# Optimization experiments

Measured on AMD Instinct MI355X. Metric: run time of the kernel, lower is better.

Reference implementation:

```python
import jax, jax.numpy as jnp
import numpy as np

CAPS_N, DIMS_N, ROUNDS = 10, 16, 3
IN_CAPS_N, IN_DIMS_N = 1152, 8
BATCH = 256
EPS = 1e-7  # keras backend.epsilon()


def squash(x, axis=-1):
    sq = jnp.sum(x * x, axis=axis, keepdims=True)
    return (sq / (1.0 + sq)) * x / jnp.sqrt(sq + EPS)


def setup_inputs() -> dict:
    key = jax.random.key(0)
    k1, k2 = jax.random.split(key)
    inputs = jax.random.normal(k1, (BATCH, IN_CAPS_N, IN_DIMS_N), dtype=jnp.float32)
    # glorot-ish scale for the transform weights
    W = jax.random.normal(k2, (CAPS_N, IN_CAPS_N, DIMS_N, IN_DIMS_N), dtype=jnp.float32) * 0.05
    return {"inputs": inputs, "W": W}


def reference(inputs, W):
    # u_hat[b,j,i,d] = W[j,i] @ inputs[b,i]  (per-pair prediction vectors)
    u_hat = jnp.einsum('jide,bie->bjid', W, inputs)  # [B, caps_n, in_caps_n, dims_n]
    B = inputs.shape[0]
    cc = jnp.zeros((B, CAPS_N, IN_CAPS_N), dtype=u_hat.dtype)  # routing logits
    v = None
    for r in range(ROUNDS):
        c = jax.nn.softmax(cc, axis=1)                    # softmax over output capsules
        s = jnp.einsum('bji,bjid->bjd', c, u_hat)         # weighted sum over input caps
        v = squash(s, axis=-1)                            # [B, caps_n, dims_n]
        if r != ROUNDS - 1:
            cc = cc + jnp.einsum('bjid,bjd->bji', u_hat, v)  # agreement
    return v
```

## Files before the change

### kernel.cpp

```cpp
#include <hip/hip_runtime.h>

#define B_N 256
#define IC_N 1152
#define J_N 10
#define D_N 16

typedef __attribute__((ext_vector_type(8))) short short8;
typedef __attribute__((ext_vector_type(4))) float floatx4;

union u4s8 { uint4 u; short8 s; };

__device__ __forceinline__ float bf_lo(unsigned int u){
  union { unsigned int i; float f; } c; c.i = u << 16; return c.f;
}
__device__ __forceinline__ float bf_hi(unsigned int u){
  union { unsigned int i; float f; } c; c.i = u & 0xffff0000u; return c.f;
}
__device__ __forceinline__ unsigned int rne16(float f){
  union { float ff; unsigned int i; } c; c.ff = f;
  return (c.i + 0x7FFFu + ((c.i >> 16) & 1u)) >> 16;
}
__device__ __forceinline__ unsigned int pack_rne(float lo, float hi){
  return rne16(lo) | (rne16(hi) << 16);
}
__device__ __forceinline__ unsigned int pack_trunc(float lo, float hi){
  union { float f; unsigned int u; } a, b; a.f = lo; b.f = hi;
  return __builtin_amdgcn_perm(b.u, a.u, 0x07060302u);
}

__global__ __launch_bounds__(256) void caps_prep(
    const float* __restrict__ W, const float* __restrict__ x,
    uint4* __restrict__ wsf, uint4* __restrict__ wcc2,
    uint4* __restrict__ xbf_ib, uint4* __restrict__ xbf_bi,
    float* __restrict__ vsum)
{
  const int tid = threadIdx.x;
  if (blockIdx.x < 720) {
    __shared__ unsigned int lw[1024];
    const int j = blockIdx.x / 72, itile = blockIdx.x % 72;
    const float4* Wt = (const float4*)(W + ((size_t)(j * IC_N + itile * 16) << 7));
    #pragma unroll
    for (int h = 0; h < 2; ++h) {
      const float4 f = Wt[h * 256 + tid];
      lw[(h * 256 + tid) * 2]     = pack_rne(f.x, f.y);
      lw[(h * 256 + tid) * 2 + 1] = pack_rne(f.z, f.w);
    }
    __syncthreads();
    {
      const int ktl = tid >> 6, lane = tid & 63;
      const int base = (ktl * 4 + (lane >> 4)) * 64 + (lane & 15) * 4;
      uint4 q;
      q.x = lw[base]; q.y = lw[base + 1]; q.z = lw[base + 2]; q.w = lw[base + 3];
      wsf[((size_t)j * 288 + itile * 4 + ktl) * 64 + lane] = q;
    }
    {
      const int e = tid >> 5, lane2 = tid & 31;
      const int il = lane2 & 15, dbase = (lane2 >> 4) * 8;
      unsigned short h[8];
      #pragma unroll
      for (int k = 0; k < 8; ++k) {
        const unsigned int u = lw[il * 64 + (dbase + k) * 4 + (e >> 1)];
        h[k] = (e & 1) ? (unsigned short)(u >> 16) : (unsigned short)(u & 0xffffu);
      }
      uint4 q;
      q.x = h[0] | ((unsigned int)h[1] << 16);
      q.y = h[2] | ((unsigned int)h[3] << 16);
      q.z = h[4] | ((unsigned int)h[5] << 16);
      q.w = h[6] | ((unsigned int)h[7] << 16);
      wcc2[(((size_t)j * 8 + e) * 72 + itile) * 32 + lane2] = q;
    }
  } else {
    __shared__ unsigned int tx[4][64 * 17];
    const int xb = blockIdx.x - 720;
    const int t0 = xb * 256 + tid;
    if (t0 < B_N * J_N * D_N) vsum[t0] = 0.f;
    const int b0 = (xb / 18) * 16;
    const int i0 = (xb % 18) * 64;
    #pragma unroll
    for (int r = 0; r < 4; ++r) {
      const int bl = r * 4 + (tid >> 6);
      const int il = tid & 63;
      const float4* sp = (const float4*)(x + ((size_t)((b0 + bl) * IC_N + i0 + il) << 3));
      const float4 a = sp[0], c = sp[1];
      uint4 q;
      q.x = pack_rne(a.x, a.y); q.y = pack_rne(a.z, a.w);
      q.z = pack_rne(c.x, c.y); q.w = pack_rne(c.z, c.w);
      xbf_bi[(size_t)(b0 + bl) * IC_N + i0 + il] = q;
      tx[0][il * 17 + bl] = q.x; tx[1][il * 17 + bl] = q.y;
      tx[2][il * 17 + bl] = q.z; tx[3][il * 17 + bl] = q.w;
    }
    __syncthreads();
    #pragma unroll
    for (int it = 0; it < 4; ++it) {
      const int p  = it * 256 + tid;
      const int il = p >> 4, bl = p & 15;
      uint4 q;
      q.x = tx[0][il * 17 + bl]; q.y = tx[1][il * 17 + bl];
      q.z = tx[2][il * 17 + bl]; q.w = tx[3][il * 17 + bl];
      xbf_ib[(size_t)(i0 + il) * 256 + b0 + bl] = q;
    }
  }
}

__global__ __launch_bounds__(640, 5) void caps_pass(
    const uint4* __restrict__ xbf_ib,
    const uint4* __restrict__ xbf_bi,
    const uint4* __restrict__ wsf,
    const uint4* __restrict__ wcc2,
    const uint4* __restrict__ vsbf,
    float* __restrict__ s_part,
    const int round)
{
  __shared__ float ccl[10 * 16 * 17];

  const int tid  = threadIdx.x;
  const int wave = tid >> 6;
  const int lane = tid & 63;
  const int quad = lane >> 4;
  const int col  = lane & 15;
  const int b0   = blockIdx.x << 4;
  const int i0   = blockIdx.y << 4;

  if (round > 0) {
    short8 av = {0,0,0,0,0,0,0,0};
    if (quad < 2)
      av = *(const short8*)&vsbf[((size_t)(b0 + col) * J_N + wave) * 2 + quad];

    uint4 bvq[8];
    #pragma unroll
    for (int e = 0; e < 8; ++e) {
      uint4 q = {0u, 0u, 0u, 0u};
      if (lane < 32)
        q = wcc2[(((size_t)wave * 8 + e) * 72 + blockIdx.y) * 32 + lane];
      bvq[e] = q;
    }
    uint4 xr[4];
    #pragma unroll
    for (int r = 0; r < 4; ++r)
      xr[r] = xbf_bi[(size_t)(b0 + quad * 4 + r) * IC_N + i0 + col];

    floatx4 cc4 = {0.f, 0.f, 0.f, 0.f};
    #pragma unroll
    for (int e = 0; e < 8; ++e) {
      u4s8 bv; bv.u = bvq[e];
      floatx4 tf = {0.f, 0.f, 0.f, 0.f};
      tf = __builtin_amdgcn_mfma_f32_16x16x32_bf16(av, bv.s, tf, 0, 0, 0);
      #pragma unroll
      for (int r = 0; r < 4; ++r) {
        const unsigned int u = ((const unsigned int*)&xr[r])[e >> 1];
        const float xe = (e & 1) ? bf_hi(u) : bf_lo(u);
        cc4[r] += tf[r] * xe;
      }
    }
    #pragma unroll
    for (int r = 0; r < 4; ++r)
      ccl[(wave * 16 + col) * 17 + quad * 4 + r] = cc4[r];
    __syncthreads();
    if (tid < 256) {
      const int i = tid >> 4, b = tid & 15;
      float cc[10];
      #pragma unroll
      for (int j = 0; j < 10; ++j) cc[j] = ccl[(j * 16 + i) * 17 + b];
      float m = cc[0];
      #pragma unroll
      for (int j = 1; j < 10; ++j) m = fmaxf(m, cc[j]);
      float den = 0.f;
      #pragma unroll
      for (int j = 0; j < 10; ++j) { cc[j] = __expf(cc[j] - m); den += cc[j]; }
      const float rd = __builtin_amdgcn_rcpf(den);
      #pragma unroll
      for (int j = 0; j < 10; ++j) ccl[(j * 16 + i) * 17 + b] = cc[j] * rd;
    }
    __syncthreads();
  }

  floatx4 acc = {0.f, 0.f, 0.f, 0.f};
  uint4 xq[4], wf[4];
  float cv[4];
  #pragma unroll
  for (int kt = 0; kt < 4; ++kt) {
    const int il = kt * 4 + quad;
    xq[kt] = xbf_ib[(size_t)(i0 + il) * 256 + b0 + col];
    wf[kt] = wsf[((size_t)wave * 288 + (blockIdx.y << 2) + kt) * 64 + lane];
    cv[kt] = (round > 0) ? ccl[(wave * 16 + il) * 17 + col] : 0.1f;
  }
  #pragma unroll
  for (int kt = 0; kt < 4; ++kt) {
    short8 af;
    unsigned int* aq = (unsigned int*)&af;
    aq[0] = pack_trunc(bf_lo(xq[kt].x) * cv[kt], bf_hi(xq[kt].x) * cv[kt]);
    aq[1] = pack_trunc(bf_lo(xq[kt].y) * cv[kt], bf_hi(xq[kt].y) * cv[kt]);
    aq[2] = pack_trunc(bf_lo(xq[kt].z) * cv[kt], bf_hi(xq[kt].z) * cv[kt]);
    aq[3] = pack_trunc(bf_lo(xq[kt].w) * cv[kt], bf_hi(xq[kt].w) * cv[kt]);
    u4s8 bw; bw.u = wf[kt];
    acc = __builtin_amdgcn_mfma_f32_16x16x32_bf16(af, bw.s, acc, 0, 0, 0);
  }
  float* sp = s_part + ((((size_t)blockIdx.x * 10 + wave) * 16 + quad * 4) * 72
                        + blockIdx.y) * 16 + col;
  #pragma unroll
  for (int r = 0; r < 4; ++r) sp[(size_t)r * 72 * 16] = acc[r];
}

__global__ __launch_bounds__(256) void caps_squash(
    const float* __restrict__ s_part, float* __restrict__ vsum,
    unsigned int* __restrict__ vsbf_u, float* __restrict__ out, const int round)
{
  const int tid  = threadIdx.x;
  const int w    = tid >> 6;
  const int lane = tid & 63;
  const int bj   = blockIdx.x * 4 + w;
  const int b    = bj / 10, j = bj - b * 10;
  const int btile = b >> 4, brem = b & 15;
  const float* base = s_part + (((size_t)btile * 10 + j) * 16 + brem) * 1152;
  float acc = 0.f;
  #pragma unroll
  for (int q = 0; q < 18; ++q) acc += base[q * 64 + lane];
  acc += __shfl_xor(acc, 16, 64);
  acc += __shfl_xor(acc, 32, 64);
  const float s = acc;
  float sq = s * s;
  sq += __shfl_xor(sq, 1, 16);
  sq += __shfl_xor(sq, 2, 16);
  sq += __shfl_xor(sq, 4, 16);
  sq += __shfl_xor(sq, 8, 16);
  const float coef = (sq / (1.f + sq)) * rsqrtf(sq + 1e-7f);
  const float v = coef * s;
  if (round < 2) {
    const float vprev = (lane < 16) ? vsum[bj * 16 + lane] : 0.f;
    const float vt = vprev + v;
    const float vtn = __shfl_down(vt, 1, 64);
    if (lane < 16) {
      vsum[bj * 16 + lane] = vt;
      if (!(lane & 1))
        vsbf_u[bj * 8 + (lane >> 1)] = pack_rne(vt, vtn);
    }
  } else if (lane < 16) {
    out[bj * 16 + lane] = v;
  }
}

extern "C" void kernel_launch(void* const* d_in, const int* in_sizes, int n_in,
                              void* d_out, int out_size, void* d_ws, size_t ws_size,
                              hipStream_t stream)
{
  const float* x = (const float*)d_in[0];
  const float* W = (const float*)d_in[1];

  uint4* wsf    = (uint4*)d_ws;
  uint4* wcc2   = wsf + 184320;
  uint4* xbf_ib = wcc2 + 184320;
  uint4* xbf_bi = xbf_ib + 294912;
  float* s_prt  = (float*)(xbf_bi + 294912);
  float* vsum   = s_prt + 2949120;
  unsigned int* vsbf_u = (unsigned int*)(vsum + 40960);

  caps_prep<<<dim3(1008), dim3(256), 0, stream>>>(W, x, wsf, wcc2,
                                                  xbf_ib, xbf_bi, vsum);
  for (int r = 0; r < 3; ++r) {
    caps_pass<<<dim3(16, 72), dim3(640), 0, stream>>>(
        xbf_ib, xbf_bi, wsf, wcc2, (const uint4*)vsbf_u, s_prt, r);
    caps_squash<<<dim3(640), dim3(256), 0, stream>>>(
        s_prt, vsum, vsbf_u, (float*)d_out, r);
  }
}
```

Measured before the change: 115.8 us.

## Fuse squash into routing pass via last-block ticket and double i-tile size

Merges the per-round pass and squash kernels into a single kernel. Each block now covers 32 input capsules instead of 16, which halves the grid and the partial-sum buffer. After storing partials, blocks take a ticket from an atomic counter; the last 64 blocks spin until all 576 blocks have arrived, then do the reduction and squash. This removes three kernel launches and halves the reduction traffic. In exchange it relies on the spin-wait: it deadlocks if the finishing blocks cannot be resident while earlier blocks are still pending, and it adds atomic overhead.

Result: slower. 167.4 us (+44.5%).

```diff
diff --git a/kernel.cpp b/kernel.cpp
--- a/kernel.cpp
+++ b/kernel.cpp
@@ -4,6 +4,8 @@
 #define IC_N 1152
 #define J_N 10
 #define D_N 16
+#define NBLK 576
+#define NWORK 64
 
 typedef __attribute__((ext_vector_type(8))) short short8;
 typedef __attribute__((ext_vector_type(4))) float floatx4;
@@ -32,9 +34,10 @@
     const float* __restrict__ W, const float* __restrict__ x,
     uint4* __restrict__ wsf, uint4* __restrict__ wcc2,
     uint4* __restrict__ xbf_ib, uint4* __restrict__ xbf_bi,
-    float* __restrict__ vsum)
+    float* __restrict__ vsum, unsigned int* __restrict__ cnt)
 {
   const int tid = threadIdx.x;
+  if (blockIdx.x == 1007 && tid < 4) cnt[tid] = 0u;
   if (blockIdx.x < 720) {
     __shared__ unsigned int lw[1024];
     const int j = blockIdx.x / 72, itile = blockIdx.x % 72;
@@ -47,11 +50,11 @@
     }
     __syncthreads();
     {
-      const int ktl = tid >> 6, lane = tid & 63;
-      const int base = (ktl * 4 + (lane >> 4)) * 64 + (lane & 15) * 4;
+      const int ktl = tid >> 6, ln = tid & 63;
+      const int base = (ktl * 4 + (ln >> 4)) * 64 + (ln & 15) * 4;
       uint4 q;
       q.x = lw[base]; q.y = lw[base + 1]; q.z = lw[base + 2]; q.w = lw[base + 3];
-      wsf[((size_t)j * 288 + itile * 4 + ktl) * 64 + lane] = q;
+      wsf[((size_t)j * 288 + itile * 4 + ktl) * 64 + ln] = q;
     }
     {
       const int e = tid >> 5, lane2 = tid & 31;
@@ -102,16 +105,15 @@
   }
 }
 
-__global__ __launch_bounds__(640, 5) void caps_pass(
-    const uint4* __restrict__ xbf_ib,
-    const uint4* __restrict__ xbf_bi,
-    const uint4* __restrict__ wsf,
-    const uint4* __restrict__ wcc2,
-    const uint4* __restrict__ vsbf,
-    float* __restrict__ s_part,
-    const int round)
+__global__ __launch_bounds__(640, 6) void caps_round(
+    const uint4* __restrict__ xbf_ib, const uint4* __restrict__ xbf_bi,
+    const uint4* __restrict__ wsf, const uint4* __restrict__ wcc2,
+    const uint4* __restrict__ vsbf, float* __restrict__ s_part,
+    float* __restrict__ vsum, unsigned int* __restrict__ vsbf_u,
+    float* __restrict__ out, unsigned int* __restrict__ cnt, const int round)
 {
-  __shared__ float ccl[10 * 16 * 17];
+  __shared__ float ccl[10 * 32 * 17];
+  __shared__ int tick_s;
 
   const int tid  = threadIdx.x;
   const int wave = tid >> 6;
@@ -119,48 +121,51 @@
   const int quad = lane >> 4;
   const int col  = lane & 15;
   const int b0   = blockIdx.x << 4;
-  const int i0   = blockIdx.y << 4;
+  const int i0   = blockIdx.y << 5;
 
   if (round > 0) {
     short8 av = {0,0,0,0,0,0,0,0};
     if (quad < 2)
       av = *(const short8*)&vsbf[((size_t)(b0 + col) * J_N + wave) * 2 + quad];
 
-    uint4 bvq[8];
-    #pragma unroll
-    for (int e = 0; e < 8; ++e) {
-      uint4 q = {0u, 0u, 0u, 0u};
-      if (lane < 32)
-        q = wcc2[(((size_t)wave * 8 + e) * 72 + blockIdx.y) * 32 + lane];
-      bvq[e] = q;
-    }
-    uint4 xr[4];
-    #pragma unroll
-    for (int r = 0; r < 4; ++r)
-      xr[r] = xbf_bi[(size_t)(b0 + quad * 4 + r) * IC_N + i0 + col];
-
-    floatx4 cc4 = {0.f, 0.f, 0.f, 0.f};
-    #pragma unroll
-    for (int e = 0; e < 8; ++e) {
-      u4s8 bv; bv.u = bvq[e];
-      floatx4 tf = {0.f, 0.f, 0.f, 0.f};
-      tf = __builtin_amdgcn_mfma_f32_16x16x32_bf16(av, bv.s, tf, 0, 0, 0);
-      #pragma unroll
-      for (int r = 0; r < 4; ++r) {
-        const unsigned int u = ((const unsigned int*)&xr[r])[e >> 1];
-        const float xe = (e & 1) ? bf_hi(u) : bf_lo(u);
-        cc4[r] += tf[r] * xe;
+    #pragma unroll
+    for (int t2 = 0; t2 < 2; ++t2) {
+      uint4 bvq[8];
+      #pragma unroll
+      for (int e = 0; e < 8; ++e) {
+        uint4 q = {0u, 0u, 0u, 0u};
+        if (lane < 32)
+          q = wcc2[(((size_t)wave * 8 + e) * 72 + (blockIdx.y << 1) + t2) * 32 + lane];
+        bvq[e] = q;
       }
-    }
-    #pragma unroll
-    for (int r = 0; r < 4; ++r)
-      ccl[(wave * 16 + col) * 17 + quad * 4 + r] = cc4[r];
-    __syncthreads();
-    if (tid < 256) {
+      uint4 xr[4];
+      #pragma unroll
+      for (int r = 0; r < 4; ++r)
+        xr[r] = xbf_bi[(size_t)(b0 + quad * 4 + r) * IC_N + i0 + t2 * 16 + col];
+
+      floatx4 cc4 = {0.f, 0.f, 0.f, 0.f};
+      #pragma unroll
+      for (int e = 0; e < 8; ++e) {
+        u4s8 bv; bv.u = bvq[e];
+        floatx4 tf = {0.f, 0.f, 0.f, 0.f};
+        tf = __builtin_amdgcn_mfma_f32_16x16x32_bf16(av, bv.s, tf, 0, 0, 0);
+        #pragma unroll
+        for (int r = 0; r < 4; ++r) {
+          const unsigned int u = ((const unsigned int*)&xr[r])[e >> 1];
+          const float xe = (e & 1) ? bf_hi(u) : bf_lo(u);
+          cc4[r] += tf[r] * xe;
+        }
+      }
+      #pragma unroll
+      for (int r = 0; r < 4; ++r)
+        ccl[(wave * 32 + t2 * 16 + col) * 17 + quad * 4 + r] = cc4[r];
+    }
+    __syncthreads();
+    if (tid < 512) {
       const int i = tid >> 4, b = tid & 15;
       float cc[10];
       #pragma unroll
-      for (int j = 0; j < 10; ++j) cc[j] = ccl[(j * 16 + i) * 17 + b];
+      for (int j = 0; j < 10; ++j) cc[j] = ccl[(j * 32 + i) * 17 + b];
       float m = cc[0];
       #pragma unroll
       for (int j = 1; j < 10; ++j) m = fmaxf(m, cc[j]);
@@ -169,55 +174,71 @@
       for (int j = 0; j < 10; ++j) { cc[j] = __expf(cc[j] - m); den += cc[j]; }
       const float rd = __builtin_amdgcn_rcpf(den);
       #pragma unroll
-      for (int j = 0; j < 10; ++j) ccl[(j * 16 + i) * 17 + b] = cc[j] * rd;
+      for (int j = 0; j < 10; ++j) ccl[(j * 32 + i) * 17 + b] = cc[j] * rd;
     }
     __syncthreads();
   }
 
   floatx4 acc = {0.f, 0.f, 0.f, 0.f};
-  uint4 xq[4], wf[4];
-  float cv[4];
   #pragma unroll
-  for (int kt = 0; kt < 4; ++kt) {
-    const int il = kt * 4 + quad;
-    xq[kt] = xbf_ib[(size_t)(i0 + il) * 256 + b0 + col];
-    wf[kt] = wsf[((size_t)wave * 288 + (blockIdx.y << 2) + kt) * 64 + lane];
-    cv[kt] = (round > 0) ? ccl[(wave * 16 + il) * 17 + col] : 0.1f;
-  }
+  for (int g = 0; g < 2; ++g) {
+    uint4 xq[4], wf[4];
+    float cv[4];
+    #pragma unroll
+    for (int k = 0; k < 4; ++k) {
+      const int kt = g * 4 + k;
+      const int il = kt * 4 + quad;
+      xq[k] = xbf_ib[(size_t)(i0 + il) * 256 + b0 + col];
+      wf[k] = wsf[((size_t)wave * 288 + (blockIdx.y << 3) + kt) * 64 + lane];
+      cv[k] = (round > 0) ? ccl[(wave * 32 + il) * 17 + col] : 0.1f;
+    }
+    #pragma unroll
+    for (int k = 0; k < 4; ++k) {
+      short8 af;
+      unsigned int* aq = (unsigned int*)&af;
+      aq[0] = pack_trunc(bf_lo(xq[k].x) * cv[k], bf_hi(xq[k].x) * cv[k]);
+      aq[1] = pack_trunc(bf_lo(xq[k].y) * cv[k], bf_hi(xq[k].y) * cv[k]);
+      aq[2] = pack_trunc(bf_lo(xq[k].z) * cv[k], bf_hi(xq[k].z) * cv[k]);
+      aq[3] = pack_trunc(bf_lo(xq[k].w) * cv[k], bf_hi(xq[k].w) * cv[k]);
+      u4s8 bw; bw.u = wf[k];
+      acc = __builtin_amdgcn_mfma_f32_16x16x32_bf16(af, bw.s, acc, 0, 0, 0);
+    }
+  }
+  {
+    float* sp = s_part + ((((size_t)blockIdx.x * 10 + wave) * 16 + quad * 4) * 36
+                          + blockIdx.y) * 16 + col;
+    #pragma unroll
+    for (int rr = 0; rr < 4; ++rr)
+      __hip_atomic_store(&sp[rr * 576], acc[rr],
+                         __ATOMIC_RELAXED, __HIP_MEMORY_SCOPE_AGENT);
+  }
+
+  __syncthreads();
+  if (tid == 0)
+    tick_s = (int)__hip_atomic_fetch_add(&cnt[round], 1u,
+                                         __ATOMIC_ACQ_REL, __HIP_MEMORY_SCOPE_AGENT);
+  __syncthreads();
+  const int ticket = tick_s;
+  if (ticket < NBLK - NWORK) return;
+  const int wid = ticket - (NBLK - NWORK);
+  if (tid == 0) {
+    while (__hip_atomic_load(&cnt[round], __ATOMIC_ACQUIRE,
+                             __HIP_MEMORY_SCOPE_AGENT) < NBLK)
+      __builtin_amdgcn_s_sleep(8);
+  }
+  __syncthreads();
+
+  const int bjl = tid >> 4;
+  const int d   = tid & 15;
+  const int bj  = wid * 40 + bjl;
+  const int b = bj / 10, j = bj - b * 10;
+  const int btile = b >> 4, brem = b & 15;
+  float* basep = s_part + ((((size_t)btile * 10 + j) * 16 + brem) * 36) * 16 + d;
+  float s = 0.f;
   #pragma unroll
-  for (int kt = 0; kt < 4; ++kt) {
-    short8 af;
-    unsigned int* aq = (unsigned int*)&af;
-    aq[0] = pack_trunc(bf_lo(xq[kt].x) * cv[kt], bf_hi(xq[kt].x) * cv[kt]);
-    aq[1] = pack_trunc(bf_lo(xq[kt].y) * cv[kt], bf_hi(xq[kt].y) * cv[kt]);
-    aq[2] = pack_trunc(bf_lo(xq[kt].z) * cv[kt], bf_hi(xq[kt].z) * cv[kt]);
-    aq[3] = pack_trunc(bf_lo(xq[kt].w) * cv[kt], bf_hi(xq[kt].w) * cv[kt]);
-    u4s8 bw; bw.u = wf[kt];
-    acc = __builtin_amdgcn_mfma_f32_16x16x32_bf16(af, bw.s, acc, 0, 0, 0);
-  }
-  float* sp = s_part + ((((size_t)blockIdx.x * 10 + wave) * 16 + quad * 4) * 72
-                        + blockIdx.y) * 16 + col;
-  #pragma unroll
-  for (int r = 0; r < 4; ++r) sp[(size_t)r * 72 * 16] = acc[r];
-}
-
-__global__ __launch_bounds__(256) void caps_squash(
-    const float* __restrict__ s_part, float* __restrict__ vsum,
-    unsigned int* __restrict__ vsbf_u, float* __restrict__ out, const int round)
-{
-  const int tid  = threadIdx.x;
-  const int w    = tid >> 6;
-  const int lane = tid & 63;
-  const int bj   = blockIdx.x * 4 + w;
-  const int b    = bj / 10, j = bj - b * 10;
-  const int btile = b >> 4, brem = b & 15;
-  const float* base = s_part + (((size_t)btile * 10 + j) * 16 + brem) * 1152;
-  float acc = 0.f;
-  #pragma unroll
-  for (int q = 0; q < 18; ++q) acc += base[q * 64 + lane];
-  acc += __shfl_xor(acc, 16, 64);
-  acc += __shfl_xor(acc, 32, 64);
-  const float s = acc;
+  for (int ch = 0; ch < 36; ++ch)
+    s += __hip_atomic_load(&basep[ch * 16], __ATOMIC_RELAXED,
+                           __HIP_MEMORY_SCOPE_AGENT);
   float sq = s * s;
   sq += __shfl_xor(sq, 1, 16);
   sq += __shfl_xor(sq, 2, 16);
@@ -226,16 +247,12 @@
   const float coef = (sq / (1.f + sq)) * rsqrtf(sq + 1e-7f);
   const float v = coef * s;
   if (round < 2) {
-    const float vprev = (lane < 16) ? vsum[bj * 16 + lane] : 0.f;
-    const float vt = vprev + v;
+    const float vt = vsum[bj * 16 + d] + v;
     const float vtn = __shfl_down(vt, 1, 64);
-    if (lane < 16) {
-      vsum[bj * 16 + lane] = vt;
-      if (!(lane & 1))
-        vsbf_u[bj * 8 + (lane >> 1)] = pack_rne(vt, vtn);
-    }
-  } else if (lane < 16) {
-    out[bj * 16 + lane] = v;
+    vsum[bj * 16 + d] = vt;
+    if (!(d & 1)) vsbf_u[bj * 8 + (d >> 1)] = pack_rne(vt, vtn);
+  } else {
+    out[bj * 16 + d] = v;
   }
 }
 
@@ -243,23 +260,24 @@
                               void* d_out, int out_size, void* d_ws, size_t ws_size,
                               hipStream_t stream)
 {
-  const float* x = (const float*)d_in[0];
-  const float* W = (const float*)d_in[1];
+  const float* x_p = (const float*)d_in[0];
+  const float* W_p = (const float*)d_in[1];
 
   uint4* wsf    = (uint4*)d_ws;
   uint4* wcc2   = wsf + 184320;
   uint4* xbf_ib = wcc2 + 184320;
   uint4* xbf_bi = xbf_ib + 294912;
   float* s_prt  = (float*)(xbf_bi + 294912);
-  float* vsum   = s_prt + 2949120;
+  float* vsum   = s_prt + 1474560;
   unsigned int* vsbf_u = (unsigned int*)(vsum + 40960);
-
-  caps_prep<<<dim3(1008), dim3(256), 0, stream>>>(W, x, wsf, wcc2,
-                                                  xbf_ib, xbf_bi, vsum);
+  unsigned int* cnt    = vsbf_u + 20480;
+  float* out_p  = (float*)d_out;
+
+  caps_prep<<<dim3(1008), dim3(256), 0, stream>>>(W_p, x_p, wsf, wcc2,
+                                                  xbf_ib, xbf_bi, vsum, cnt);
   for (int r = 0; r < 3; ++r) {
-    caps_pass<<<dim3(16, 72), dim3(640), 0, stream>>>(
-        xbf_ib, xbf_bi, wsf, wcc2, (const uint4*)vsbf_u, s_prt, r);
-    caps_squash<<<dim3(640), dim3(256), 0, stream>>>(
-        s_prt, vsum, vsbf_u, (float*)d_out, r);
-  }
-}
+    caps_round<<<dim3(16, 36), dim3(640), 0, stream>>>(
+        xbf_ib, xbf_bi, wsf, wcc2, (const uint4*)vsbf_u, s_prt,
+        vsum, vsbf_u, out_p, cnt, r);
+  }
+}
```
